# Kernel tuning notes

Measured on AMD Instinct MI355X. Metric: run time of the kernel, lower is better.

## Reference

```python
import jax, jax.numpy as jnp
import numpy as np

D = 64      # d_model == initialFeatureSize
H = 8       # n_heads
F2 = D + 2  # hidden_size + 2


def _ln(x, g, b):
    m = x.mean(-1, keepdims=True)
    v = ((x - m) ** 2).mean(-1, keepdims=True)
    return (x - m) / jnp.sqrt(v + 1e-5) * g + b


def _mask_weights(idx):
    # softmax of where(idx>0, 1, -9e15) along axis 1 -> mean over non-pad slots
    return jax.nn.softmax(jnp.where(idx > 0, 1.0, -9e15), axis=1)


def _tblock(x, mask, qkv, Wo, bo, ln, ffW, ffb):
    # standard masked multi-head self-attention block (eval mode, dropout off)
    B, L, Dm = x.shape
    dh = Dm // H
    q = (x @ qkv[0]).reshape(B, L, H, dh)
    k = (x @ qkv[1]).reshape(B, L, H, dh)
    v = (x @ qkv[2]).reshape(B, L, H, dh)
    s = jnp.einsum('blhd,bmhd->bhlm', q, k) / jnp.sqrt(jnp.asarray(dh, x.dtype))
    s = jnp.where(mask[:, None, None, :], -1e9, s)
    ctx = jnp.einsum('bhlm,bmhd->blhd', jax.nn.softmax(s, -1), v).reshape(B, L, Dm)
    x = _ln(x + ctx @ Wo + bo, ln[0, 0], ln[0, 1])
    ff = jax.nn.relu(x @ ffW[0] + ffb[0]) @ ffW[1] + ffb[1]
    return _ln(x + ff, ln[1, 0], ln[1, 1])


def _forward(user_emb, global_cen_emb, local_time_emb, cas_pos_emb, local_inf_emb,
             hgnn_w1, hgnn_w2, hgnn_w3, text_lin_W, text_lin_b,
             weight, weight2, fus_l1_W, fus_l1_b, fus_l2_W, fus_l2_b, out_W, out_b,
             tb_qkv, tb_Wo, tb_bo, tb_ln, tb_ff_W, tb_ff_b,
             text2emb, spread_status,
             data_idx, seq, timestamps, user_level, useq, user_inf, user_cen):
    # --- dead code kept for faithfulness (result unused) ---
    w3n = hgnn_w3 / jnp.linalg.norm(hgnn_w3, axis=1, keepdims=True)
    _tw = (w3n @ w3n.T).mean()
    t = text2emb @ text_lin_W + text_lin_b
    _t = ((t - t.min()) / (t.max() - t.min()) * 999).astype(jnp.int32)
    # --- HGNN layer: gather -> masked mean -> relu -> gather -> masked mean ---
    x = (user_emb + global_cen_emb[user_cen]) @ hgnn_w1            # [N, D]
    edge = jax.nn.relu(jnp.einsum('nlc,nl->nc', x[seq], _mask_weights(seq)))  # [E, D]
    node = jnp.einsum('umc,um->uc', (edge @ hgnn_w2)[useq], _mask_weights(useq))  # [N, D]
    # --- batch gather for attention branches ---
    seq_b = seq[data_idx]                                          # [B, L]
    w_b = _mask_weights(seq_b)
    att_mask = seq_b == 0                                          # PAD == 0
    adj = node[seq_b]                                              # [B, L, D]
    # temporal branch
    h_t = adj + local_time_emb[timestamps[data_idx]]
    o_t = _tblock(h_t, att_mask, tb_qkv[0], tb_Wo[0], tb_bo[0], tb_ln[0], tb_ff_W[0], tb_ff_b[0])
    n_t = jnp.einsum('blc,bl->bc', o_t, w_b)
    n_t = jnp.concatenate([n_t, spread_status[data_idx][:, 2:] / 3600.0 / 24.0], -1) @ weight
    # structural branch
    h_s = adj + local_inf_emb[user_inf[data_idx]] + cas_pos_emb[user_level[data_idx]]
    o_s = _tblock(h_s, att_mask, tb_qkv[1], tb_Wo[1], tb_bo[1], tb_ln[1], tb_ff_W[1], tb_ff_b[1])
    n_s = jnp.einsum('blc,bl->bc', o_s, w_b)
    n_s = jnp.concatenate([n_s, spread_status[data_idx][:, :2]], -1) @ weight2
    # gated fusion
    emb = jnp.stack([n_t, n_s])                                    # [2, B, F2]
    score = jax.nn.softmax(jnp.tanh(emb @ fus_l1_W + fus_l1_b) @ fus_l2_W + fus_l2_b, axis=0)
    fused = (score * emb).sum(0)
    return jax.nn.log_softmax(fused @ out_W + out_b, axis=1)       # [B, 2]


def setup_inputs() -> dict:
    key = jax.random.key(0)
    ks = iter(jax.random.split(key, 48))
    N, E, L, M, B, EMB = 100000, 20000, 50, 20, 1024, 300
    stdv = 1.0 / np.sqrt(D)
    u = lambda shape: jax.random.uniform(next(ks), shape, jnp.float32, -stdv, stdv)
    ri = lambda shape, hi: jax.random.randint(next(ks), shape, 0, hi, jnp.int32)
    ln_init = jnp.broadcast_to(jnp.stack([jnp.ones(D), jnp.zeros(D)])[None, None], (2, 2, 2, D))
    return dict(
        user_emb=u((N, D)), global_cen_emb=u((600, D)), local_time_emb=u((5000, D)),
        cas_pos_emb=u((50, D)), local_inf_emb=u((200, D)),
        hgnn_w1=u((D, D)), hgnn_w2=u((D, D)), hgnn_w3=u((100, EMB)),
        text_lin_W=u((EMB, 200)), text_lin_b=u((200,)),
        weight=u((F2, F2)), weight2=u((F2, F2)),
        fus_l1_W=u((F2, F2)), fus_l1_b=u((F2,)), fus_l2_W=u((F2, 1)), fus_l2_b=u((1,)),
        out_W=u((F2, 2)), out_b=u((2,)),
        tb_qkv=u((2, 3, D, D)), tb_Wo=u((2, D, D)), tb_bo=u((2, D)),
        tb_ln=jnp.array(ln_init),
        tb_ff_W=u((2, 2, D, D)), tb_ff_b=u((2, 2, D)),
        text2emb=jax.random.normal(next(ks), (E, EMB), jnp.float32),
        spread_status=jax.random.uniform(next(ks), (E, 4), jnp.float32, 0.0, 100.0),
        data_idx=ri((B,), E), seq=ri((E, L), N), timestamps=ri((E, L), 5000),
        user_level=ri((E, L), 50), useq=ri((N, M), E), user_inf=ri((E, L), 200),
        user_cen=ri((N,), 600),
    )


def reference(user_emb, global_cen_emb, local_time_emb, cas_pos_emb, local_inf_emb,
              hgnn_w1, hgnn_w2, hgnn_w3, text_lin_W, text_lin_b,
              weight, weight2, fus_l1_W, fus_l1_b, fus_l2_W, fus_l2_b, out_W, out_b,
              tb_qkv, tb_Wo, tb_bo, tb_ln, tb_ff_W, tb_ff_b,
              text2emb, spread_status,
              data_idx, seq, timestamps, user_level, useq, user_inf, user_cen):
    return _forward(user_emb, global_cen_emb, local_time_emb, cas_pos_emb, local_inf_emb,
                    hgnn_w1, hgnn_w2, hgnn_w3, text_lin_W, text_lin_b,
                    weight, weight2, fus_l1_W, fus_l1_b, fus_l2_W, fus_l2_b, out_W, out_b,
                    tb_qkv, tb_Wo, tb_bo, tb_ln, tb_ff_W, tb_ff_b,
                    text2emb, spread_status,
                    data_idx, seq, timestamps, user_level, useq, user_inf, user_cen)
```

## Files before the change

### kernel.cpp

```cpp
#include <hip/hip_runtime.h>
#include <hip/hip_bf16.h>

#define D  64
#define L  50
#define M  20
#define BB 1024
#define F2 66
#define NEDGE 20000
#define NUSER 100000

typedef __attribute__((ext_vector_type(8))) short bf16x8;
typedef __attribute__((ext_vector_type(4))) float f32x4;

#define MFMA(a,b,c) __builtin_amdgcn_mfma_f32_16x16x32_bf16(a,b,c,0,0,0)

__device__ __forceinline__ short f2bf(float f) {
    union { __hip_bfloat16 h; unsigned short u; } cv;
    cv.h = __float2bfloat16(f);
    return (short)cv.u;
}
__device__ __forceinline__ uint32_t pk2(float a, float b) {
    union { __hip_bfloat162 h; uint32_t u; } cv;
    cv.h.x = __float2bfloat16(a);
    cv.h.y = __float2bfloat16(b);
    return cv.u;
}
__device__ __forceinline__ float bf2f(short s) {
    return __uint_as_float(((uint32_t)(unsigned short)s) << 16);
}
__device__ __forceinline__ float bf2fu(unsigned short s) {
    return __uint_as_float(((uint32_t)s) << 16);
}
__device__ __forceinline__ int swz(int row, int col) {
    return row * 64 + (col ^ ((row & 7) << 3));
}
__device__ __forceinline__ float wsum(float v) {
    #pragma unroll
    for (int off = 32; off > 0; off >>= 1) v += __shfl_xor(v, off);
    return v;
}


__global__ __launch_bounds__(256) void k_prep(
    const float* __restrict__ qkv, const float* __restrict__ Wo,
    const float* __restrict__ ffW, const float* __restrict__ w2,
    const float* __restrict__ w1, short* __restrict__ wb)
{
    int idx = blockIdx.x * 256 + threadIdx.x;
    int mat = idx >> 12, e = idx & 4095;
    int c = e >> 6, k = e & 63;
    const float* src;
    if (mat == 13)      src = w1;
    else if (mat == 12) src = w2;
    else {
        int bi = mat / 6, m = mat % 6;
        if (m < 3)       src = qkv + ((size_t)bi * 3 + m) * 4096;
        else if (m == 3) src = Wo + (size_t)bi * 4096;
        else             src = ffW + ((size_t)bi * 2 + (m - 4)) * 4096;
    }
    wb[(size_t)mat * 4096 + c * 64 + k] = f2bf(src[k * 64 + c]);
}


__global__ __launch_bounds__(256) void k_hgnn1m(
    const float* __restrict__ user_emb, const float* __restrict__ cen_emb,
    const int* __restrict__ user_cen, const short* __restrict__ w1t,
    unsigned short* __restrict__ xb)
{
    const int tid = threadIdx.x, lane = tid & 63, lo = lane & 15, hg = lane >> 4, w = tid >> 6;
    const int row0 = blockIdx.x * 64 + 16 * w;
    const int arow = row0 + lo;
    const bool av = arow < NUSER;
    const int cidx = av ? user_cen[arow] : 0;

    f32x4 acc[4];
    #pragma unroll
    for (int c = 0; c < 4; ++c) { acc[c][0] = acc[c][1] = acc[c][2] = acc[c][3] = 0.f; }

    #pragma unroll
    for (int ks = 0; ks < 2; ++ks) {
        bf16x8 a;
        if (av) {
            const float4 u0 = *(const float4*)&user_emb[(size_t)arow * 64 + 32 * ks + 8 * hg];
            const float4 u1 = *(const float4*)&user_emb[(size_t)arow * 64 + 32 * ks + 8 * hg + 4];
            const float4 c0 = *(const float4*)&cen_emb[(size_t)cidx * 64 + 32 * ks + 8 * hg];
            const float4 c1 = *(const float4*)&cen_emb[(size_t)cidx * 64 + 32 * ks + 8 * hg + 4];
            uint32_t p0 = pk2(u0.x + c0.x, u0.y + c0.y);
            uint32_t p1 = pk2(u0.z + c0.z, u0.w + c0.w);
            uint32_t p2 = pk2(u1.x + c1.x, u1.y + c1.y);
            uint32_t p3 = pk2(u1.z + c1.z, u1.w + c1.w);
            union { uint32_t u[4]; bf16x8 v; } af;
            af.u[0] = p0; af.u[1] = p1; af.u[2] = p2; af.u[3] = p3;
            a = af.v;
        } else {
            #pragma unroll
            for (int i = 0; i < 8; ++i) a[i] = 0;
        }
        #pragma unroll
        for (int c = 0; c < 4; ++c) {
            bf16x8 bb = *(const bf16x8*)(w1t + (16 * c + lo) * 64 + 32 * ks + 8 * hg);
            acc[c] = MFMA(a, bb, acc[c]);
        }
    }
    #pragma unroll
    for (int c = 0; c < 4; ++c) {
        #pragma unroll
        for (int r = 0; r < 4; ++r) {
            int row = row0 + 4 * hg + r;
            if (row < NUSER) xb[(size_t)row * 64 + 16 * c + lo] = (unsigned short)f2bf(acc[c][r]);
        }
    }
}


__global__ __launch_bounds__(256) void k_edge_gather(
    const unsigned short* __restrict__ xb, const int* __restrict__ seq,
    unsigned short* __restrict__ em)
{
    const int j = threadIdx.x & 63;
    const int e = blockIdx.x * 4 + (threadIdx.x >> 6);
    const int s = j >> 4, g = j & 15;
    int my = (j < L) ? seq[(size_t)e * L + j] : 0;
    int cnt = (int)__popcll(__ballot(j < L && my > 0));
    float wv = cnt ? 1.f / (float)cnt : 1.f / (float)L;
    uint2 tv[13];
    bool use[13];
    #pragma unroll
    for (int i = 0; i < 13; ++i) {
        int r = 4 * i + s;
        int rr = (r < L) ? r : 0;
        int idx = __shfl(my, rr);
        use[i] = (r < L) && (cnt ? (idx > 0) : true);
        tv[i] = *(const uint2*)&xb[(size_t)idx * D + 4 * g];
    }
    float a0 = 0.f, a1 = 0.f, a2 = 0.f, a3 = 0.f;
    #pragma unroll
    for (int i = 0; i < 13; ++i) {
        uint32_t lw = tv[i].x, hw = tv[i].y;
        a0 += use[i] ? bf2fu((unsigned short)(lw & 0xffff)) : 0.f;
        a1 += use[i] ? bf2fu((unsigned short)(lw >> 16))    : 0.f;
        a2 += use[i] ? bf2fu((unsigned short)(hw & 0xffff)) : 0.f;
        a3 += use[i] ? bf2fu((unsigned short)(hw >> 16))    : 0.f;
    }
    a0 += __shfl_xor(a0, 16); a0 += __shfl_xor(a0, 32);
    a1 += __shfl_xor(a1, 16); a1 += __shfl_xor(a1, 32);
    a2 += __shfl_xor(a2, 16); a2 += __shfl_xor(a2, 32);
    a3 += __shfl_xor(a3, 16); a3 += __shfl_xor(a3, 32);
    if (s == 0) {
        uint2 o;
        o.x = pk2(fmaxf(a0 * wv, 0.f), fmaxf(a1 * wv, 0.f));
        o.y = pk2(fmaxf(a2 * wv, 0.f), fmaxf(a3 * wv, 0.f));
        *(uint2*)&em[(size_t)e * D + 4 * g] = o;
    }
}


__global__ __launch_bounds__(256) void k_gemm_edge(
    const unsigned short* __restrict__ em, const short* __restrict__ w2t,
    unsigned short* __restrict__ e2b)
{
    const int tid = threadIdx.x, lane = tid & 63, lo = lane & 15, hg = lane >> 4, w = tid >> 6;
    const int row0 = blockIdx.x * 64 + 16 * w;
    bf16x8 zf;
    #pragma unroll
    for (int i = 0; i < 8; ++i) zf[i] = 0;
    f32x4 acc[4];
    #pragma unroll
    for (int c = 0; c < 4; ++c) { acc[c][0] = acc[c][1] = acc[c][2] = acc[c][3] = 0.f; }
    #pragma unroll
    for (int ks = 0; ks < 2; ++ks) {
        bf16x8 a = zf;
        if (row0 + lo < NEDGE)
            a = *(const bf16x8*)&em[(size_t)(row0 + lo) * D + 32 * ks + 8 * hg];
        #pragma unroll
        for (int c = 0; c < 4; ++c) {
            bf16x8 bb = *(const bf16x8*)(w2t + (16 * c + lo) * 64 + 32 * ks + 8 * hg);
            acc[c] = MFMA(a, bb, acc[c]);
        }
    }
    #pragma unroll
    for (int c = 0; c < 4; ++c) {
        #pragma unroll
        for (int r = 0; r < 4; ++r) {
            int row = row0 + 4 * hg + r;
            if (row < NEDGE) e2b[(size_t)row * D + 16 * c + lo] = (unsigned short)f2bf(acc[c][r]);
        }
    }
}


__global__ __launch_bounds__(256) void k_nodem(
    const unsigned short* __restrict__ e2b, const int* __restrict__ seq,
    const int* __restrict__ useq, const int* __restrict__ data_idx,
    unsigned short* __restrict__ nb)
{
    const int j = threadIdx.x & 63;
    const int w = threadIdx.x >> 6;
    const int p = blockIdx.x * 4 + w;
    const int b = p / L, l = p - b * L;
    const int ib = data_idx[b];
    const int u = seq[(size_t)ib * L + l];
    const int s = j >> 4, g = j & 15;
    int my = (j < M) ? useq[(size_t)u * M + j] : 0;
    int cnt = (int)__popcll(__ballot(j < M && my > 0));
    float wv = cnt ? 1.f / (float)cnt : 1.f / (float)M;
    uint2 tv[5];
    bool use[5];
    #pragma unroll
    for (int i = 0; i < 5; ++i) {
        int r = 4 * i + s;
        int idx = __shfl(my, r);
        use[i] = cnt ? (idx > 0) : true;
        tv[i] = *(const uint2*)&e2b[(size_t)idx * D + 4 * g];
    }
    float a0 = 0.f, a1 = 0.f, a2 = 0.f, a3 = 0.f;
    #pragma unroll
    for (int i = 0; i < 5; ++i) {
        uint32_t lw = tv[i].x, hw = tv[i].y;
        a0 += use[i] ? bf2fu((unsigned short)(lw & 0xffff)) : 0.f;
        a1 += use[i] ? bf2fu((unsigned short)(lw >> 16))    : 0.f;
        a2 += use[i] ? bf2fu((unsigned short)(hw & 0xffff)) : 0.f;
        a3 += use[i] ? bf2fu((unsigned short)(hw >> 16))    : 0.f;
    }
    a0 += __shfl_xor(a0, 16); a0 += __shfl_xor(a0, 32);
    a1 += __shfl_xor(a1, 16); a1 += __shfl_xor(a1, 32);
    a2 += __shfl_xor(a2, 16); a2 += __shfl_xor(a2, 32);
    a3 += __shfl_xor(a3, 16); a3 += __shfl_xor(a3, 32);
    if (s == 0) {
        uint2 o;
        o.x = pk2(a0 * wv, a1 * wv);
        o.y = pk2(a2 * wv, a3 * wv);
        *(uint2*)&nb[(size_t)p * D + 4 * g] = o;
    }
}

#define XB 0
#define QB 3328
#define KB 6656
#define VBT 9984
#define BRO 14080
#define PB  28160

__global__ __launch_bounds__(512, 4) void k_tblock2(
    const unsigned short* __restrict__ nb,
    const int* __restrict__ seq, const int* __restrict__ data_idx,
    const int* __restrict__ timestamps, const int* __restrict__ user_inf,
    const int* __restrict__ user_level,
    const float* __restrict__ time_emb, const float* __restrict__ inf_emb,
    const float* __restrict__ pos_emb,
    const short* __restrict__ wb,
    const float* __restrict__ bo_all, const float* __restrict__ ln_all,
    const float* __restrict__ ffb_all, const float* __restrict__ spread,
    const float* __restrict__ weight, const float* __restrict__ weight2,
    float* __restrict__ n_t, float* __restrict__ n_s)
{
    const int tid = threadIdx.x;
    const int lane = tid & 63, lo = lane & 15, hg = lane >> 4, w = tid >> 6;
    const int b = blockIdx.x;
    const int ib = data_idx[b];

    __shared__ __align__(16) short sm[36352];
    __shared__ float nbuf[2][4][64];
    __shared__ float nvec[2][F2];
    __shared__ int   seqi[52];

    for (int i = tid; i < 1600; i += 512) {
        int row = i >> 5, cp = (i & 31) * 2;
        uint32_t nn = *(const uint32_t*)(nb + (size_t)b * 3200 + row * 64 + cp);
        float n0 = bf2fu((unsigned short)(nn & 0xffff));
        float n1 = bf2fu((unsigned short)(nn >> 16));
        int ts  = timestamps[(size_t)ib * L + row];
        int inf = user_inf[(size_t)ib * L + row];
        int lev = user_level[(size_t)ib * L + row];
        float2 te = *(const float2*)(time_emb + (size_t)ts * 64 + cp);
        float2 ie = *(const float2*)(inf_emb + (size_t)inf * 64 + cp);
        float2 pe = *(const float2*)(pos_emb + (size_t)lev * 64 + cp);
        *(uint32_t*)&sm[XB + swz(row, cp)]       = pk2(n0 + te.x, n1 + te.y);
        *(uint32_t*)&sm[BRO + XB + swz(row, cp)] = pk2(n0 + ie.x + pe.x, n1 + ie.y + pe.y);
    }
    if (tid < 52) seqi[tid] = (tid < 50) ? seq[(size_t)ib * L + tid] : 0;
    {
        for (int i = tid; i < 448; i += 512) {
            ((int*)(sm + XB + 50 * 64))[i] = 0;
            ((int*)(sm + QB + 50 * 64))[i] = 0;
            ((int*)(sm + KB + 50 * 64))[i] = 0;
            ((int*)(sm + BRO + XB + 50 * 64))[i] = 0;
            ((int*)(sm + BRO + QB + 50 * 64))[i] = 0;
            ((int*)(sm + BRO + KB + 50 * 64))[i] = 0;
        }
    }
    __syncthreads();

    #pragma unroll
    for (int t3 = 0; t3 < 3; ++t3) {
        int task = w + 8 * t3;
        int br  = (task >= 12) ? 1 : 0;
        int rem = task - 12 * br;
        int mat = rem >> 2, rt = rem & 3;
        const int RB = br * BRO;
        const short* WTb = wb + (size_t)br * 6 * 4096 + (size_t)mat * 4096;
        f32x4 a4[4];
        #pragma unroll
        for (int c = 0; c < 4; ++c) { a4[c][0] = a4[c][1] = a4[c][2] = a4[c][3] = 0.f; }
        #pragma unroll
        for (int ks = 0; ks < 2; ++ks) {
            bf16x8 xa = *(const bf16x8*)&sm[RB + XB + swz(16 * rt + lo, 32 * ks + 8 * hg)];
            #pragma unroll
            for (int c = 0; c < 4; ++c) {
                bf16x8 bb = *(const bf16x8*)(WTb + (16 * c + lo) * 64 + 32 * ks + 8 * hg);
                a4[c] = MFMA(xa, bb, a4[c]);
            }
        }
        if (mat == 0) {
            #pragma unroll
            for (int c = 0; c < 4; ++c)
                #pragma unroll
                for (int r = 0; r < 4; ++r) {
                    int row = 16 * rt + 4 * hg + r;
                    if (row < 52)
                        sm[RB + QB + swz(row, 16 * c + lo)] = f2bf(a4[c][r] * 0.35355339059327378f);
                }
        } else if (mat == 1) {
            #pragma unroll
            for (int c = 0; c < 4; ++c)
                #pragma unroll
                for (int r = 0; r < 4; ++r) {
                    int row = 16 * rt + 4 * hg + r;
                    if (row < 52) sm[RB + KB + swz(row, 16 * c + lo)] = f2bf(a4[c][r]);
                }
        } else {
            #pragma unroll
            for (int c = 0; c < 4; ++c)
                #pragma unroll
                for (int r = 0; r < 4; ++r) {
                    int row = 16 * rt + 4 * hg + r, col = 16 * c + lo;
                    sm[RB + VBT + swz(col, row)] = (row < 50) ? f2bf(a4[c][r]) : (short)0;
                }
        }
    }
    __syncthreads();

    int svl = (lane < 50) ? seqi[lane] : 0;
    int cnt = (int)__popcll(__ballot(svl > 0));
    float msel[4][4];
    #pragma unroll
    for (int mt = 0; mt < 4; ++mt) {
        #pragma unroll
        for (int r = 0; r < 4; ++r) {
            int m = 16 * mt + 4 * hg + r;
            msel[mt][r] = (m < 50) ? ((seqi[m] > 0) ? 0.f : -1e9f) : -3.0e38f;
        }
    }

    bf16x8 zf;
    #pragma unroll
    for (int i = 0; i < 8; ++i) zf[i] = 0;

    f32x4 ctx2[2][4];
    const int hd = w;
    const int pbase = PB + (w << 10);
    #pragma unroll
    for (int br = 0; br < 2; ++br) {
        const int RB = br * BRO;
        bf16x8 ka[4], qf[4];
        #pragma unroll
        for (int t = 0; t < 4; ++t) {
            ka[t] = zf; qf[t] = zf;
            if (hg == 0) {
                ka[t] = *(const bf16x8*)&sm[RB + KB + swz(16 * t + lo, hd * 8)];
                qf[t] = *(const bf16x8*)&sm[RB + QB + swz(16 * t + lo, hd * 8)];
            }
        }
        f32x4 s[4][4];
        __builtin_amdgcn_s_setprio(1);
        #pragma unroll
        for (int mt = 0; mt < 4; ++mt) {
            #pragma unroll
            for (int c = 0; c < 4; ++c) {
                f32x4 z; z[0] = z[1] = z[2] = z[3] = 0.f;
                s[mt][c] = MFMA(ka[mt], qf[c], z);
            }
        }
        __builtin_amdgcn_s_setprio(0);
        #pragma unroll
        for (int mt = 0; mt < 4; ++mt) {
            #pragma unroll
            for (int r = 0; r < 4; ++r) {
                float ms = msel[mt][r];
                bool valid = (ms == 0.f);
                #pragma unroll
                for (int c = 0; c < 4; ++c) s[mt][c][r] = valid ? s[mt][c][r] : ms;
            }
        }
        uint32_t pk[4][4][2];
        #pragma unroll
        for (int c = 0; c < 4; ++c) {
            float mx = -3.4e38f;
            #pragma unroll
            for (int mt = 0; mt < 4; ++mt) {
                #pragma unroll
                for (int r = 0; r < 4; ++r) mx = fmaxf(mx, s[mt][c][r]);
            }
            mx = fmaxf(mx, __shfl_xor(mx, 16));
            mx = fmaxf(mx, __shfl_xor(mx, 32));
            float den = 0.f;
            #pragma unroll
            for (int mt = 0; mt < 4; ++mt) {
                #pragma unroll
                for (int r = 0; r < 4; ++r) {
                    float e = __expf(s[mt][c][r] - mx);
                    s[mt][c][r] = e; den += e;
                }
            }
            den += __shfl_xor(den, 16);
            den += __shfl_xor(den, 32);
            float inv = 1.f / den;
            #pragma unroll
            for (int mt = 0; mt < 4; ++mt) {
                pk[mt][c][0] = pk2(s[mt][c][0] * inv, s[mt][c][1] * inv);
                pk[mt][c][1] = pk2(s[mt][c][2] * inv, s[mt][c][3] * inv);
            }
        }
        #pragma unroll
        for (int t = 0; t < 4; ++t) {
            ctx2[br][t][0] = ctx2[br][t][1] = ctx2[br][t][2] = ctx2[br][t][3] = 0.f;
        }
        __builtin_amdgcn_s_setprio(1);
        #pragma unroll
        for (int rt = 0; rt < 4; ++rt) {
            #pragma unroll
            for (int mt = 0; mt < 4; ++mt) {
                int m0 = 16 * mt + 4 * hg;
                int sa = pbase + (lo << 6) + (m0 ^ ((lo & 7) << 3));
                uint2 pv; pv.x = pk[mt][rt][0]; pv.y = pk[mt][rt][1];
                *(uint2*)&sm[sa] = pv;
            }
            #pragma unroll
            for (int ks = 0; ks < 2; ++ks) {
                int ra = pbase + (lo << 6) + ((32 * ks + 8 * hg) ^ ((lo & 7) << 3));
                bf16x8 af = *(const bf16x8*)&sm[ra];
                bf16x8 bfr = zf;
                if (lo < 8) bfr = *(const bf16x8*)&sm[RB + VBT + swz(hd * 8 + lo, 32 * ks + 8 * hg)];
                ctx2[br][rt] = MFMA(af, bfr, ctx2[br][rt]);
            }
        }
        __builtin_amdgcn_s_setprio(0);
    }
    __syncthreads();
    if (lo < 8) {
        #pragma unroll
        for (int br = 0; br < 2; ++br) {
            const int RB = br * BRO;
            #pragma unroll
            for (int rt = 0; rt < 4; ++rt) {
                #pragma unroll
                for (int r = 0; r < 4; ++r) {
                    int row = 16 * rt + 4 * hg + r;
                    if (row < 52) sm[RB + KB + swz(row, hd * 8 + lo)] = f2bf(ctx2[br][rt][r]);
                }
            }
        }
    }
    __syncthreads();

    {
        const int ebr = w >> 2, ws = w & 3;
        const int RB = ebr * BRO;
        const short* WT  = wb + (size_t)ebr * 6 * 4096;
        const float* bo  = bo_all + ebr * 64;
        const float* lnp = ln_all + ebr * 256;
        const float* ffb = ffb_all + ebr * 128;

        float g1[4], b1[4], g2[4], b2[4], boc[4], f1b[4], f2b[4];
        #pragma unroll
        for (int c = 0; c < 4; ++c) {
            int col = 16 * c + lo;
            g1[c] = lnp[col];        b1[c] = lnp[64 + col];
            g2[c] = lnp[128 + col];  b2[c] = lnp[192 + col];
            boc[c] = bo[col]; f1b[c] = ffb[col]; f2b[c] = ffb[64 + col];
        }

        f32x4 acc[4];
        #pragma unroll
        for (int c = 0; c < 4; ++c) { acc[c][0] = acc[c][1] = acc[c][2] = acc[c][3] = 0.f; }
        #pragma unroll
        for (int ks = 0; ks < 2; ++ks) {
            bf16x8 a = *(const bf16x8*)&sm[RB + KB + swz(16 * ws + lo, 32 * ks + 8 * hg)];
            #pragma unroll
            for (int c = 0; c < 4; ++c) {
                bf16x8 bb = *(const bf16x8*)(WT + 3 * 4096 + (16 * c + lo) * 64 + 32 * ks + 8 * hg);
                acc[c] = MFMA(a, bb, acc[c]);
            }
        }
        float x1v[4][4];
        #pragma unroll
        for (int r = 0; r < 4; ++r) {
            int row = 16 * ws + 4 * hg + r;
            float t0 = bf2f(sm[RB + XB + swz(row, lo)])      + acc[0][r] + boc[0];
            float t1 = bf2f(sm[RB + XB + swz(row, 16 + lo)]) + acc[1][r] + boc[1];
            float t2 = bf2f(sm[RB + XB + swz(row, 32 + lo)]) + acc[2][r] + boc[2];
            float t3 = bf2f(sm[RB + XB + swz(row, 48 + lo)]) + acc[3][r] + boc[3];
            float s1 = t0 + t1 + t2 + t3;
            float q1 = t0 * t0 + t1 * t1 + t2 * t2 + t3 * t3;
            #pragma unroll
            for (int d = 1; d <= 8; d <<= 1) { s1 += __shfl_xor(s1, d); q1 += __shfl_xor(q1, d); }
            float mean = s1 * 0.015625f;
            float var = q1 * 0.015625f - mean * mean;
            float rin = rsqrtf(var + 1e-5f);
            float x0 = (t0 - mean) * rin * g1[0] + b1[0];
            float x1 = (t1 - mean) * rin * g1[1] + b1[1];
            float x2 = (t2 - mean) * rin * g1[2] + b1[2];
            float x3 = (t3 - mean) * rin * g1[3] + b1[3];
            x1v[0][r] = x0; x1v[1][r] = x1; x1v[2][r] = x2; x1v[3][r] = x3;
            if (row < 52) {
                sm[RB + QB + swz(row, lo)]      = f2bf(x0);
                sm[RB + QB + swz(row, 16 + lo)] = f2bf(x1);
                sm[RB + QB + swz(row, 32 + lo)] = f2bf(x2);
                sm[RB + QB + swz(row, 48 + lo)] = f2bf(x3);
            }
        }
        #pragma unroll
        for (int c = 0; c < 4; ++c) { acc[c][0] = acc[c][1] = acc[c][2] = acc[c][3] = 0.f; }
        #pragma unroll
        for (int ks = 0; ks < 2; ++ks) {
            bf16x8 a = *(const bf16x8*)&sm[RB + QB + swz(16 * ws + lo, 32 * ks + 8 * hg)];
            #pragma unroll
            for (int c = 0; c < 4; ++c) {
                bf16x8 bb = *(const bf16x8*)(WT + 4 * 4096 + (16 * c + lo) * 64 + 32 * ks + 8 * hg);
                acc[c] = MFMA(a, bb, acc[c]);
            }
        }
        #pragma unroll
        for (int c = 0; c < 4; ++c) {
            #pragma unroll
            for (int r = 0; r < 4; ++r) {
                int row = 16 * ws + 4 * hg + r;
                if (row < 52) sm[RB + KB + swz(row, 16 * c + lo)] = f2bf(fmaxf(acc[c][r] + f1b[c], 0.f));
            }
        }
        #pragma unroll
        for (int c = 0; c < 4; ++c) { acc[c][0] = acc[c][1] = acc[c][2] = acc[c][3] = 0.f; }
        #pragma unroll
        for (int ks = 0; ks < 2; ++ks) {
            bf16x8 a = *(const bf16x8*)&sm[RB + KB + swz(16 * ws + lo, 32 * ks + 8 * hg)];
            #pragma unroll
            for (int c = 0; c < 4; ++c) {
                bf16x8 bb = *(const bf16x8*)(WT + 5 * 4096 + (16 * c + lo) * 64 + 32 * ks + 8 * hg);
                acc[c] = MFMA(a, bb, acc[c]);
            }
        }
        float wv = (cnt > 0) ? 1.f / (float)cnt : 0.02f;
        float np[4] = {0.f, 0.f, 0.f, 0.f};
        #pragma unroll
        for (int r = 0; r < 4; ++r) {
            int row = 16 * ws + 4 * hg + r;
            float t0 = x1v[0][r] + acc[0][r] + f2b[0];
            float t1 = x1v[1][r] + acc[1][r] + f2b[1];
            float t2 = x1v[2][r] + acc[2][r] + f2b[2];
            float t3 = x1v[3][r] + acc[3][r] + f2b[3];
            float s1 = t0 + t1 + t2 + t3;
            float q1 = t0 * t0 + t1 * t1 + t2 * t2 + t3 * t3;
            #pragma unroll
            for (int d = 1; d <= 8; d <<= 1) { s1 += __shfl_xor(s1, d); q1 += __shfl_xor(q1, d); }
            float mean = s1 * 0.015625f;
            float var = q1 * 0.015625f - mean * mean;
            float rin = rsqrtf(var + 1e-5f);
            float wl = 0.f;
            if (row < 50) {
                int sv = seqi[row];
                wl = (cnt > 0) ? ((sv > 0) ? wv : 0.f) : wv;
            }
            np[0] += ((t0 - mean) * rin * g2[0] + b2[0]) * wl;
            np[1] += ((t1 - mean) * rin * g2[1] + b2[1]) * wl;
            np[2] += ((t2 - mean) * rin * g2[2] + b2[2]) * wl;
            np[3] += ((t3 - mean) * rin * g2[3] + b2[3]) * wl;
        }
        #pragma unroll
        for (int c = 0; c < 4; ++c) {
            np[c] += __shfl_xor(np[c], 16);
            np[c] += __shfl_xor(np[c], 32);
        }
        if (hg == 0) {
            #pragma unroll
            for (int c = 0; c < 4; ++c) nbuf[ebr][ws][16 * c + lo] = np[c];
        }
    }
    __syncthreads();
    if (tid < 64)
        nvec[0][tid] = nbuf[0][0][tid] + nbuf[0][1][tid] + nbuf[0][2][tid] + nbuf[0][3][tid];
    else if (tid < 128)
        nvec[1][tid - 64] = nbuf[1][0][tid - 64] + nbuf[1][1][tid - 64] +
                            nbuf[1][2][tid - 64] + nbuf[1][3][tid - 64];
    else if (tid == 128) nvec[0][64] = spread[(size_t)ib * 4 + 2] * (1.f / 86400.f);
    else if (tid == 129) nvec[0][65] = spread[(size_t)ib * 4 + 3] * (1.f / 86400.f);
    else if (tid == 130) nvec[1][64] = spread[(size_t)ib * 4 + 0];
    else if (tid == 131) nvec[1][65] = spread[(size_t)ib * 4 + 1];
    __syncthreads();
    if (tid < F2) {
        float a = 0.f;
        for (int k = 0; k < F2; ++k) a += nvec[0][k] * weight[k * F2 + tid];
        n_t[(size_t)b * F2 + tid] = a;
    } else if (tid >= 128 && tid < 128 + F2) {
        int col = tid - 128;
        float a = 0.f;
        for (int k = 0; k < F2; ++k) a += nvec[1][k] * weight2[k * F2 + col];
        n_s[(size_t)b * F2 + col] = a;
    }
}


__global__ __launch_bounds__(256) void k_fuse(
    const float* __restrict__ n_t, const float* __restrict__ n_s,
    const float* __restrict__ l1W, const float* __restrict__ l1b,
    const float* __restrict__ l2W, const float* __restrict__ l2b,
    const float* __restrict__ outW, const float* __restrict__ outb,
    float* __restrict__ out)
{
    const int w = threadIdx.x >> 6, j = threadIdx.x & 63;
    const int b = blockIdx.x * 4 + w;
    __shared__ float et[4][F2], es[4][F2], fused[4][F2];
    for (int t = j; t < F2; t += 64) { et[w][t] = n_t[(size_t)b * F2 + t]; es[w][t] = n_s[(size_t)b * F2 + t]; }
    float sl[2];
    for (int s = 0; s < 2; ++s) {
        const float* e = s ? es[w] : et[w];
        float part = 0.f;
        for (int t = j; t < F2; t += 64) {
            float acc = l1b[t];
            for (int k = 0; k < F2; ++k) acc += e[k] * l1W[k * F2 + t];
            part += tanhf(acc) * l2W[t];
        }
        part = wsum(part);
        sl[s] = part + l2b[0];
    }
    float mx = fmaxf(sl[0], sl[1]);
    float e0 = __expf(sl[0] - mx), e1 = __expf(sl[1] - mx);
    float inv = 1.f / (e0 + e1);
    float sc0 = e0 * inv, sc1 = e1 * inv;
    for (int t = j; t < F2; t += 64) fused[w][t] = sc0 * et[w][t] + sc1 * es[w][t];
    float p0 = 0.f, p1 = 0.f;
    for (int t = j; t < F2; t += 64) {
        p0 += fused[w][t] * outW[t * 2 + 0];
        p1 += fused[w][t] * outW[t * 2 + 1];
    }
    p0 = wsum(p0); p1 = wsum(p1);
    if (j == 0) {
        float l0 = p0 + outb[0], l1v = p1 + outb[1];
        float m = fmaxf(l0, l1v);
        float lse = m + logf(__expf(l0 - m) + __expf(l1v - m));
        out[(size_t)b * 2 + 0] = l0 - lse;
        out[(size_t)b * 2 + 1] = l1v - lse;
    }
}

extern "C" void kernel_launch(void* const* d_in, const int* in_sizes, int n_in,
                              void* d_out, int out_size, void* d_ws, size_t ws_size,
                              hipStream_t stream)
{
    (void)in_sizes; (void)n_in; (void)out_size; (void)ws_size;
    const float* user_emb = (const float*)d_in[0];
    const float* cen_emb  = (const float*)d_in[1];
    const float* time_emb = (const float*)d_in[2];
    const float* pos_emb  = (const float*)d_in[3];
    const float* inf_emb  = (const float*)d_in[4];
    const float* w1       = (const float*)d_in[5];
    const float* w2       = (const float*)d_in[6];
    const float* weight   = (const float*)d_in[10];
    const float* weight2  = (const float*)d_in[11];
    const float* l1W      = (const float*)d_in[12];
    const float* l1b      = (const float*)d_in[13];
    const float* l2W      = (const float*)d_in[14];
    const float* l2b      = (const float*)d_in[15];
    const float* outW     = (const float*)d_in[16];
    const float* outb     = (const float*)d_in[17];
    const float* qkv      = (const float*)d_in[18];
    const float* Wo       = (const float*)d_in[19];
    const float* bo       = (const float*)d_in[20];
    const float* lnp      = (const float*)d_in[21];
    const float* ffW      = (const float*)d_in[22];
    const float* ffb      = (const float*)d_in[23];
    const float* spread   = (const float*)d_in[25];
    const int* data_idx   = (const int*)d_in[26];
    const int* seq        = (const int*)d_in[27];
    const int* timestamps = (const int*)d_in[28];
    const int* user_level = (const int*)d_in[29];
    const int* useq       = (const int*)d_in[30];
    const int* user_inf   = (const int*)d_in[31];
    const int* user_cen   = (const int*)d_in[32];

    unsigned short* wbt = (unsigned short*)d_ws;
    unsigned short* xb  = wbt + 57344;
    unsigned short* em  = xb + 6400000;
    unsigned short* e2b = em + 1280000;
    unsigned short* nbm = e2b + 1280000;
    float* n_t = (float*)(nbm + 3276800);
    float* n_s = n_t + 67584;
    float* out = (float*)d_out;

    k_prep<<<224, 256, 0, stream>>>(qkv, Wo, ffW, w2, w1, (short*)wbt);
    k_hgnn1m<<<1563, 256, 0, stream>>>(user_emb, cen_emb, user_cen,
                                       (const short*)wbt + 13 * 4096, xb);
    k_edge_gather<<<5000, 256, 0, stream>>>(xb, seq, em);
    k_gemm_edge<<<313, 256, 0, stream>>>(em, (const short*)wbt + 12 * 4096, e2b);
    k_nodem<<<12800, 256, 0, stream>>>(e2b, seq, useq, data_idx, nbm);
    k_tblock2<<<1024, 512, 0, stream>>>(nbm, seq, data_idx, timestamps, user_inf,
                                        user_level, time_emb, inf_emb, pos_emb,
                                        (const short*)wbt, bo, lnp, ffb, spread,
                                        weight, weight2, n_t, n_s);
    k_fuse<<<256, 256, 0, stream>>>(n_t, n_s, l1W, l1b, l2W, l2b, outW, outb, out);
}
```

Measured before the change: 163.3 us.

## Double tblock workgroup to 1024 threads and shuffle P fragments in registers

The transformer-block kernel now runs 16 waves per block, so each wave handles one (branch, head) pair instead of looping over both branches. The softmax probabilities are rearranged into MFMA A-operand layout with cross-lane shuffles instead of a round trip through shared memory, which drops the per-wave P scratch region. The aim is more parallel attention work and less LDS traffic and footprint. In exchange, half the waves sit idle in the epilogue, __launch_bounds__(1024, 8) may squeeze registers, and the extra shuffles add ALU work.

```diff
diff --git a/kernel.cpp b/kernel.cpp
--- a/kernel.cpp
+++ b/kernel.cpp
@@ -239,9 +239,8 @@
 #define KB 6656
 #define VBT 9984
 #define BRO 14080
-#define PB  28160
-
-__global__ __launch_bounds__(512, 4) void k_tblock2(
+
+__global__ __launch_bounds__(1024, 8) void k_tblock2(
     const unsigned short* __restrict__ nb,
     const int* __restrict__ seq, const int* __restrict__ data_idx,
     const int* __restrict__ timestamps, const int* __restrict__ user_inf,
@@ -259,12 +258,12 @@
     const int b = blockIdx.x;
     const int ib = data_idx[b];
 
-    __shared__ __align__(16) short sm[36352];
+    __shared__ __align__(16) short sm[2 * BRO];
     __shared__ float nbuf[2][4][64];
     __shared__ float nvec[2][F2];
     __shared__ int   seqi[52];
 
-    for (int i = tid; i < 1600; i += 512) {
+    for (int i = tid; i < 1600; i += 1024) {
         int row = i >> 5, cp = (i & 31) * 2;
         uint32_t nn = *(const uint32_t*)(nb + (size_t)b * 3200 + row * 64 + cp);
         float n0 = bf2fu((unsigned short)(nn & 0xffff));
@@ -280,7 +279,7 @@
     }
     if (tid < 52) seqi[tid] = (tid < 50) ? seq[(size_t)ib * L + tid] : 0;
     {
-        for (int i = tid; i < 448; i += 512) {
+        for (int i = tid; i < 448; i += 1024) {
             ((int*)(sm + XB + 50 * 64))[i] = 0;
             ((int*)(sm + QB + 50 * 64))[i] = 0;
             ((int*)(sm + KB + 50 * 64))[i] = 0;
@@ -292,50 +291,52 @@
     __syncthreads();
 
     #pragma unroll
-    for (int t3 = 0; t3 < 3; ++t3) {
-        int task = w + 8 * t3;
-        int br  = (task >= 12) ? 1 : 0;
-        int rem = task - 12 * br;
-        int mat = rem >> 2, rt = rem & 3;
-        const int RB = br * BRO;
-        const short* WTb = wb + (size_t)br * 6 * 4096 + (size_t)mat * 4096;
-        f32x4 a4[4];
-        #pragma unroll
-        for (int c = 0; c < 4; ++c) { a4[c][0] = a4[c][1] = a4[c][2] = a4[c][3] = 0.f; }
-        #pragma unroll
-        for (int ks = 0; ks < 2; ++ks) {
-            bf16x8 xa = *(const bf16x8*)&sm[RB + XB + swz(16 * rt + lo, 32 * ks + 8 * hg)];
-            #pragma unroll
-            for (int c = 0; c < 4; ++c) {
-                bf16x8 bb = *(const bf16x8*)(WTb + (16 * c + lo) * 64 + 32 * ks + 8 * hg);
-                a4[c] = MFMA(xa, bb, a4[c]);
-            }
-        }
-        if (mat == 0) {
-            #pragma unroll
-            for (int c = 0; c < 4; ++c)
+    for (int t3 = 0; t3 < 2; ++t3) {
+        int task = w + 16 * t3;
+        if (task < 24) {
+            int br  = (task >= 12) ? 1 : 0;
+            int rem = task - 12 * br;
+            int mat = rem >> 2, rt = rem & 3;
+            const int RB = br * BRO;
+            const short* WTb = wb + (size_t)br * 6 * 4096 + (size_t)mat * 4096;
+            f32x4 a4[4];
+            #pragma unroll
+            for (int c = 0; c < 4; ++c) { a4[c][0] = a4[c][1] = a4[c][2] = a4[c][3] = 0.f; }
+            #pragma unroll
+            for (int ks = 0; ks < 2; ++ks) {
+                bf16x8 xa = *(const bf16x8*)&sm[RB + XB + swz(16 * rt + lo, 32 * ks + 8 * hg)];
                 #pragma unroll
-                for (int r = 0; r < 4; ++r) {
-                    int row = 16 * rt + 4 * hg + r;
-                    if (row < 52)
-                        sm[RB + QB + swz(row, 16 * c + lo)] = f2bf(a4[c][r] * 0.35355339059327378f);
+                for (int c = 0; c < 4; ++c) {
+                    bf16x8 bb = *(const bf16x8*)(WTb + (16 * c + lo) * 64 + 32 * ks + 8 * hg);
+                    a4[c] = MFMA(xa, bb, a4[c]);
                 }
-        } else if (mat == 1) {
-            #pragma unroll
-            for (int c = 0; c < 4; ++c)
+            }
+            if (mat == 0) {
                 #pragma unroll
-                for (int r = 0; r < 4; ++r) {
-                    int row = 16 * rt + 4 * hg + r;
-                    if (row < 52) sm[RB + KB + swz(row, 16 * c + lo)] = f2bf(a4[c][r]);
-                }
-        } else {
-            #pragma unroll
-            for (int c = 0; c < 4; ++c)
+                for (int c = 0; c < 4; ++c)
+                    #pragma unroll
+                    for (int r = 0; r < 4; ++r) {
+                        int row = 16 * rt + 4 * hg + r;
+                        if (row < 52)
+                            sm[RB + QB + swz(row, 16 * c + lo)] = f2bf(a4[c][r] * 0.35355339059327378f);
+                    }
+            } else if (mat == 1) {
                 #pragma unroll
-                for (int r = 0; r < 4; ++r) {
-                    int row = 16 * rt + 4 * hg + r, col = 16 * c + lo;
-                    sm[RB + VBT + swz(col, row)] = (row < 50) ? f2bf(a4[c][r]) : (short)0;
-                }
+                for (int c = 0; c < 4; ++c)
+                    #pragma unroll
+                    for (int r = 0; r < 4; ++r) {
+                        int row = 16 * rt + 4 * hg + r;
+                        if (row < 52) sm[RB + KB + swz(row, 16 * c + lo)] = f2bf(a4[c][r]);
+                    }
+            } else {
+                #pragma unroll
+                for (int c = 0; c < 4; ++c)
+                    #pragma unroll
+                    for (int r = 0; r < 4; ++r) {
+                        int row = 16 * rt + 4 * hg + r, col = 16 * c + lo;
+                        sm[RB + VBT + swz(col, row)] = (row < 50) ? f2bf(a4[c][r]) : (short)0;
+                    }
+            }
         }
     }
     __syncthreads();
@@ -356,12 +357,10 @@
     #pragma unroll
     for (int i = 0; i < 8; ++i) zf[i] = 0;
 
-    f32x4 ctx2[2][4];
-    const int hd = w;
-    const int pbase = PB + (w << 10);
-    #pragma unroll
-    for (int br = 0; br < 2; ++br) {
-        const int RB = br * BRO;
+    f32x4 ctx[4];
+    const int abr = w >> 3, hd = w & 7;
+    {
+        const int RB = abr * BRO;
         bf16x8 ka[4], qf[4];
         #pragma unroll
         for (int t = 0; t < 4; ++t) {
@@ -422,48 +421,42 @@
             }
         }
         #pragma unroll
-        for (int t = 0; t < 4; ++t) {
-            ctx2[br][t][0] = ctx2[br][t][1] = ctx2[br][t][2] = ctx2[br][t][3] = 0.f;
-        }
+        for (int t = 0; t < 4; ++t) { ctx[t][0] = ctx[t][1] = ctx[t][2] = ctx[t][3] = 0.f; }
         __builtin_amdgcn_s_setprio(1);
         #pragma unroll
         for (int rt = 0; rt < 4; ++rt) {
             #pragma unroll
-            for (int mt = 0; mt < 4; ++mt) {
-                int m0 = 16 * mt + 4 * hg;
-                int sa = pbase + (lo << 6) + (m0 ^ ((lo & 7) << 3));
-                uint2 pv; pv.x = pk[mt][rt][0]; pv.y = pk[mt][rt][1];
-                *(uint2*)&sm[sa] = pv;
-            }
-            #pragma unroll
             for (int ks = 0; ks < 2; ++ks) {
-                int ra = pbase + (lo << 6) + ((32 * ks + 8 * hg) ^ ((lo & 7) << 3));
-                bf16x8 af = *(const bf16x8*)&sm[ra];
+                union { uint32_t u[4]; bf16x8 v; } af;
+                #pragma unroll
+                for (int j = 0; j < 4; ++j) {
+                    int src = lo + 16 * (2 * (hg & 1) + (j >> 1));
+                    uint32_t a0 = __shfl(pk[2 * ks][rt][j & 1], src);
+                    uint32_t a1 = __shfl(pk[2 * ks + 1][rt][j & 1], src);
+                    af.u[j] = (hg < 2) ? a0 : a1;
+                }
                 bf16x8 bfr = zf;
                 if (lo < 8) bfr = *(const bf16x8*)&sm[RB + VBT + swz(hd * 8 + lo, 32 * ks + 8 * hg)];
-                ctx2[br][rt] = MFMA(af, bfr, ctx2[br][rt]);
+                ctx[rt] = MFMA(af.v, bfr, ctx[rt]);
             }
         }
         __builtin_amdgcn_s_setprio(0);
     }
     __syncthreads();
     if (lo < 8) {
-        #pragma unroll
-        for (int br = 0; br < 2; ++br) {
-            const int RB = br * BRO;
-            #pragma unroll
-            for (int rt = 0; rt < 4; ++rt) {
-                #pragma unroll
-                for (int r = 0; r < 4; ++r) {
-                    int row = 16 * rt + 4 * hg + r;
-                    if (row < 52) sm[RB + KB + swz(row, hd * 8 + lo)] = f2bf(ctx2[br][rt][r]);
-                }
+        const int RB = abr * BRO;
+        #pragma unroll
+        for (int rt = 0; rt < 4; ++rt) {
+            #pragma unroll
+            for (int r = 0; r < 4; ++r) {
+                int row = 16 * rt + 4 * hg + r;
+                if (row < 52) sm[RB + KB + swz(row, hd * 8 + lo)] = f2bf(ctx[rt][r]);
             }
         }
     }
     __syncthreads();
 
-    {
+    if (w < 8) {
         const int ebr = w >> 2, ws = w & 3;
         const int RB = ebr * BRO;
         const short* WT  = wb + (size_t)ebr * 6 * 4096;
@@ -702,9 +695,9 @@
     k_edge_gather<<<5000, 256, 0, stream>>>(xb, seq, em);
     k_gemm_edge<<<313, 256, 0, stream>>>(em, (const short*)wbt + 12 * 4096, e2b);
     k_nodem<<<12800, 256, 0, stream>>>(e2b, seq, useq, data_idx, nbm);
-    k_tblock2<<<1024, 512, 0, stream>>>(nbm, seq, data_idx, timestamps, user_inf,
-                                        user_level, time_emb, inf_emb, pos_emb,
-                                        (const short*)wbt, bo, lnp, ffb, spread,
-                                        weight, weight2, n_t, n_s);
+    k_tblock2<<<1024, 1024, 0, stream>>>(nbm, seq, data_idx, timestamps, user_inf,
+                                         user_level, time_emb, inf_emb, pos_emb,
+                                         (const short*)wbt, bo, lnp, ffb, spread,
+                                         weight, weight2, n_t, n_s);
     k_fuse<<<256, 256, 0, stream>>>(n_t, n_s, l1W, l1b, l2W, l2b, outW, outb, out);
 }
```

Measured after the change: 254.8 us. +56.1%, slower.
